# Kernel tuning notes

Measured on AMD Instinct MI355X. Metric: run time of the kernel, lower is better.

The kernel has to match this reference:

```python
import jax, jax.numpy as jnp
import numpy as np

F32 = jnp.float32
FP8_MAX = 448.0          # E4M3 max normal
MIN_NORM_EXP = -6.0      # smallest normal exponent for E4M3 (bias 7)


def _floor_log2(a):
    """Exact floor(log2(a)) for a>0 (with correction for fp rounding); 0 -> 0."""
    a_safe = jnp.where(a > 0, a, 1.0)
    e = jnp.floor(jnp.log2(a_safe))
    p = jnp.exp2(e)
    e = jnp.where(a_safe >= 2.0 * p, e + 1.0, jnp.where(a_safe < p, e - 1.0, e))
    return jax.lax.stop_gradient(e)


def quant_e4m3(x):
    """Round-to-nearest-even quantization to FP8 E4M3 (saturating, no NaN)."""
    a = jnp.abs(x)
    e = jnp.maximum(_floor_log2(a), MIN_NORM_EXP)
    step = jnp.exp2(e - 3.0)                 # mantissa ULP (3 mantissa bits)
    q = jnp.round(a / step) * step           # jnp.round = round-half-even
    q = jnp.minimum(q, FP8_MAX)
    q = jnp.where(a > 0, q, 0.0)
    return jnp.where(x < 0, -q, q)


def bits_to_float(b):
    """Decode [..., 8] spike bits (sign, e3..e0, m2..m0) to float32 E4M3 value."""
    sign = 1.0 - 2.0 * b[..., 0]
    exp = b[..., 1] * 8.0 + b[..., 2] * 4.0 + b[..., 3] * 2.0 + b[..., 4]
    man = b[..., 5] * 4.0 + b[..., 6] * 2.0 + b[..., 7]
    mag = jnp.where(exp > 0,
                    (1.0 + man / 8.0) * jnp.exp2(exp - 7.0),   # normal
                    (man / 8.0) * jnp.exp2(MIN_NORM_EXP))       # subnormal
    return sign * mag


def float_to_bits(x):
    """Encode an FP8-representable float32 into [..., 8] spike bits."""
    sgn = (x < 0).astype(F32)
    a = jnp.abs(x)
    e = jnp.clip(_floor_log2(a), MIN_NORM_EXP, 8.0)
    is_norm = a >= jnp.exp2(MIN_NORM_EXP)
    ef = jnp.where(is_norm, e + 7.0, 0.0)
    man = jnp.where(is_norm, a * jnp.exp2(-e) * 8.0 - 8.0, a * jnp.exp2(9.0))
    man = jnp.clip(jnp.round(man), 0.0, 7.0)

    def bit(v, k):
        return jnp.floor(v / (2.0 ** k)) % 2.0

    return jnp.stack([sgn,
                      bit(ef, 3), bit(ef, 2), bit(ef, 1), bit(ef, 0),
                      bit(man, 2), bit(man, 1), bit(man, 0)], axis=-1)


B, IN, OUT = 256, 512, 1024


def setup_inputs() -> dict:
    key = jax.random.key(0)
    kx, kw = jax.random.split(key)
    # random floats -> quantize to FP8 -> encode as spike bits (valid pulses)
    x_f = jax.random.normal(kx, (B, IN), F32)
    w_f = jax.random.normal(kw, (OUT, IN), F32) * (1.0 / 32.0)  # keep accum < 448
    x = float_to_bits(quant_e4m3(x_f))                 # [B, IN, 8]
    weight_pulse = float_to_bits(quant_e4m3(w_f))      # [OUT, IN, 8]
    return {"x": x, "weight_pulse": weight_pulse}


def reference(x, weight_pulse):
    # SpikeFP8Linear_Fast, mode='sequential':
    # products[i] = fp8(x_i * w_i); acc = fp8(...fp8(p0 + p1) + ... + p_{N-1})
    xf = bits_to_float(x)             # [B, IN]
    wf = bits_to_float(weight_pulse)  # [OUT, IN]

    p0 = quant_e4m3(xf[:, 0][:, None] * wf[None, :, 0])  # [B, OUT]
    xs = jnp.moveaxis(xf[:, 1:], 1, 0)  # [IN-1, B]
    ws = jnp.moveaxis(wf[:, 1:], 1, 0)  # [IN-1, OUT]

    def step(acc, xw):
        xi, wi = xw
        p = quant_e4m3(xi[:, None] * wi[None, :])
        return quant_e4m3(acc + p), None

    acc, _ = jax.lax.scan(step, p0, (xs, ws))
    return float_to_bits(acc)  # [B, OUT, 8]
```

## Files before the change

kernel.cpp:

```cpp
#include <hip/hip_runtime.h>

#define B_DIM 256
#define IN_DIM 512
#define OUT_DIM 1024

typedef __attribute__((__ext_vector_type__(2))) float v2f;

__device__ __forceinline__ float dec_pair(float4 a, float4 b) {
    int ef  = ((int)a.y << 3) | ((int)a.z << 2) | ((int)a.w << 1) | (int)b.x;
    int man = ((int)b.y << 2) | ((int)b.z << 1) | (int)b.w;
    float mag;
    if (ef > 0)
        mag = __uint_as_float(((unsigned)(ef + 120) << 23) | ((unsigned)man << 20));
    else
        mag = (float)man * 0.001953125f;
    return (a.x != 0.0f) ? -mag : mag;
}

__global__ void k_decode(const float* __restrict__ xbits,
                         const float* __restrict__ wbits,
                         float* __restrict__ xf, float* __restrict__ wt) {
    int v = blockIdx.x * 256 + threadIdx.x;
    if (v < B_DIM * IN_DIM) {
        const float4* p = (const float4*)xbits + (size_t)v * 2;
        xf[v] = dec_pair(p[0], p[1]);
    } else {
        int u = v - B_DIM * IN_DIM;
        const float4* p = (const float4*)wbits + (size_t)u * 2;
        float val = dec_pair(p[0], p[1]);
        int o = u >> 9, i = u & 511;
        wt[((size_t)(i >> 2) * OUT_DIM + o) * 4 + (i & 3)] = val;
    }
}

__device__ __forceinline__ void store8(float* __restrict__ out, int idx, float v) {
    unsigned au = __float_as_uint(v) & 0x7fffffffu;
    float sgn = (v < 0.0f) ? 1.0f : 0.0f;
    int ef, man;
    if (au >= 0x3c800000u) {
        ef  = (int)(au >> 23) - 120;
        man = (int)((au >> 20) & 7u);
    } else {
        ef  = 0;
        man = (int)(__uint_as_float(au) * 512.0f);
    }
    float4 lo = make_float4(sgn,
                            (float)((ef >> 3) & 1), (float)((ef >> 2) & 1),
                            (float)((ef >> 1) & 1));
    float4 hi = make_float4((float)(ef & 1),
                            (float)((man >> 2) & 1), (float)((man >> 1) & 1),
                            (float)(man & 1));
    float4* op = (float4*)(out + (size_t)idx * 8);
    op[0] = lo;
    op[1] = hi;
}

__global__ __launch_bounds__(256) void k_main(const float* __restrict__ xf,
                                              const float* __restrict__ wt,
                                              float* __restrict__ out) {
    int tid  = threadIdx.x;
    int lane = tid & 63;
    int wid  = tid >> 6;
    int o  = blockIdx.x * 64 + lane;
    int b0 = blockIdx.y * 8 + wid * 2;

    const float* xa = xf + (size_t)b0 * IN_DIM;
    const float* xb = xa + IN_DIM;
    const float4* wq = (const float4*)wt + o;

    v2f acc = {0.0f, 0.0f};

    float4 w0 = wq[0];
    float4 w1 = wq[(size_t)OUT_DIM];

    for (int it = 0; it < IN_DIM / 8; ++it) {
        float4 cw0 = w0, cw1 = w1;
        if (it < IN_DIM / 8 - 1) {
            w0 = wq[(size_t)(2 * it + 2) * OUT_DIM];
            w1 = wq[(size_t)(2 * it + 3) * OUT_DIM];
        }
        float wk[8]  = {cw0.x, cw0.y, cw0.z, cw0.w, cw1.x, cw1.y, cw1.z, cw1.w};
        const float* xap = xa + it * 8;
        const float* xbp = xb + it * 8;
        float xak[8], xbk[8];
#pragma unroll
        for (int k = 0; k < 8; ++k) { xak[k] = xap[k]; xbk[k] = xbp[k]; }
#pragma unroll
        for (int k = 0; k < 8; ++k) {
            float p0 = xak[k] * wk[k];
            float p1 = xbk[k] * wk[k];
            int pq = __builtin_amdgcn_cvt_pk_fp8_f32(p0, p1, 0, false);
            v2f pf = __builtin_amdgcn_cvt_pk_f32_fp8(pq, false);
            v2f s  = acc + pf;
            int sq = __builtin_amdgcn_cvt_pk_fp8_f32(s.x, s.y, 0, false);
            acc = __builtin_amdgcn_cvt_pk_f32_fp8(sq, false);
        }
    }

    store8(out, b0 * OUT_DIM + o, acc.x);
    store8(out, (b0 + 1) * OUT_DIM + o, acc.y);
}

extern "C" void kernel_launch(void* const* d_in, const int* in_sizes, int n_in,
                              void* d_out, int out_size, void* d_ws, size_t ws_size,
                              hipStream_t stream) {
    const float* xb = (const float*)d_in[0];
    const float* wb = (const float*)d_in[1];
    float* out = (float*)d_out;

    float* xf = (float*)d_ws;
    float* wt = (float*)d_ws + B_DIM * IN_DIM;

    int total = B_DIM * IN_DIM + OUT_DIM * IN_DIM;
    k_decode<<<dim3(total / 256), dim3(256), 0, stream>>>(xb, wb, xf, wt);

    dim3 grid(OUT_DIM / 64, B_DIM / 8);
    k_main<<<grid, dim3(256), 0, stream>>>(xf, wt, out);
}
```

Baseline: 101.4 us.

## Deepen weight prefetch, double-buffer x rows, scalarize row index in main loop

Replaces the single-step weight prefetch with a 4-deep rotating register pipeline, and double-buffers the x row values. It also makes the row base wave-uniform via readfirstlane so x loads can become scalar loads. Product quantization is split out of the serial accumulate chain and uses packed multiplies, so the independent work can overlap with the dependent accumulation. The prefetch reads run past the last valid weight and x rows, fetching unused data beyond the buffers, and register pressure goes up.

```diff
diff --git a/kernel.cpp b/kernel.cpp
--- a/kernel.cpp
+++ b/kernel.cpp
@@ -62,7 +62,7 @@
     int lane = tid & 63;
     int wid  = tid >> 6;
     int o  = blockIdx.x * 64 + lane;
-    int b0 = blockIdx.y * 8 + wid * 2;
+    int b0 = __builtin_amdgcn_readfirstlane(blockIdx.y * 8 + wid * 2);
 
     const float* xa = xf + (size_t)b0 * IN_DIM;
     const float* xb = xa + IN_DIM;
@@ -70,30 +70,56 @@
 
     v2f acc = {0.0f, 0.0f};
 
-    float4 w0 = wq[0];
-    float4 w1 = wq[(size_t)OUT_DIM];
-
-    for (int it = 0; it < IN_DIM / 8; ++it) {
-        float4 cw0 = w0, cw1 = w1;
-        if (it < IN_DIM / 8 - 1) {
-            w0 = wq[(size_t)(2 * it + 2) * OUT_DIM];
-            w1 = wq[(size_t)(2 * it + 3) * OUT_DIM];
-        }
-        float wk[8]  = {cw0.x, cw0.y, cw0.z, cw0.w, cw1.x, cw1.y, cw1.z, cw1.w};
-        const float* xap = xa + it * 8;
-        const float* xbp = xb + it * 8;
-        float xak[8], xbk[8];
+    float4 wA[4], wB[4];
 #pragma unroll
-        for (int k = 0; k < 8; ++k) { xak[k] = xap[k]; xbk[k] = xbp[k]; }
+    for (int d = 0; d < 4; ++d) {
+        wA[d] = wq[(size_t)(2 * d) * OUT_DIM];
+        wB[d] = wq[(size_t)(2 * d + 1) * OUT_DIM];
+    }
+    float xav[2][8], xbv[2][8];
+#pragma unroll
+    for (int d = 0; d < 2; ++d)
 #pragma unroll
         for (int k = 0; k < 8; ++k) {
-            float p0 = xak[k] * wk[k];
-            float p1 = xbk[k] * wk[k];
-            int pq = __builtin_amdgcn_cvt_pk_fp8_f32(p0, p1, 0, false);
-            v2f pf = __builtin_amdgcn_cvt_pk_f32_fp8(pq, false);
-            v2f s  = acc + pf;
-            int sq = __builtin_amdgcn_cvt_pk_fp8_f32(s.x, s.y, 0, false);
-            acc = __builtin_amdgcn_cvt_pk_f32_fp8(sq, false);
+            xav[d][k] = xa[d * 8 + k];
+            xbv[d][k] = xb[d * 8 + k];
+        }
+
+    for (int go = 0; go < 64; go += 4) {
+#pragma unroll
+        for (int ph = 0; ph < 4; ++ph) {
+            int g = go + ph;
+            float4 cwA = wA[ph], cwB = wB[ph];
+            wA[ph] = wq[(size_t)(2 * (g + 4)) * OUT_DIM];
+            wB[ph] = wq[(size_t)(2 * (g + 4) + 1) * OUT_DIM];
+
+            int xs = ph & 1;
+            float wk[8] = {cwA.x, cwA.y, cwA.z, cwA.w,
+                           cwB.x, cwB.y, cwB.z, cwB.w};
+            v2f pf[8];
+#pragma unroll
+            for (int k = 0; k < 8; ++k) {
+                v2f xp = {xav[xs][k], xbv[xs][k]};
+                v2f wv = {wk[k], wk[k]};
+                v2f p = xp * wv;
+                int pq = __builtin_amdgcn_cvt_pk_fp8_f32(p.x, p.y, 0, false);
+                pf[k] = __builtin_amdgcn_cvt_pk_f32_fp8(pq, false);
+            }
+            {
+                const float* nxa = xa + (size_t)(g + 2) * 8;
+                const float* nxb = xb + (size_t)(g + 2) * 8;
+#pragma unroll
+                for (int k = 0; k < 8; ++k) {
+                    xav[xs][k] = nxa[k];
+                    xbv[xs][k] = nxb[k];
+                }
+            }
+#pragma unroll
+            for (int k = 0; k < 8; ++k) {
+                v2f s = acc + pf[k];
+                int sq = __builtin_amdgcn_cvt_pk_fp8_f32(s.x, s.y, 0, false);
+                acc = __builtin_amdgcn_cvt_pk_f32_fp8(sq, false);
+            }
         }
     }
 
```

Result: no change. 99.60 us (-1.8%).
